# Optimization experiments

Hardware: AMD Instinct MI355X
Metric: run time of the kernel (lower is better)

## Reference

```python
import jax, jax.numpy as jnp
import numpy as np

EPS = 1e-5
LOGIT_DIM = 16   # 2**arity, arity=4
HID = 128        # circuit_hidden_dim == pe_dim
MSG = LOGIT_DIM + HID  # 144


def layer_norm(x, scale, bias):
    mu = jnp.mean(x, axis=-1, keepdims=True)
    var = jnp.mean(jnp.square(x - mu), axis=-1, keepdims=True)
    return (x - mu) * jax.lax.rsqrt(var + EPS) * scale + bias


def setup_inputs() -> dict:
    key = jax.random.key(0)
    N = 200000
    ks = jax.random.split(key, 16)
    inp = {
        'logits': jax.random.normal(ks[0], (N, LOGIT_DIM), jnp.float32),
        'hidden': jax.random.normal(ks[1], (N, HID), jnp.float32),
        'layer_pe': jax.random.normal(ks[2], (N, HID), jnp.float32),
        'intra_layer_pe': jax.random.normal(ks[3], (N, HID), jnp.float32),
        'loss': jax.random.normal(ks[4], (N,), jnp.float32),
        'layer': jax.random.randint(ks[5], (N,), 0, 8, jnp.int32),
        'sent_attributes': jax.random.normal(ks[6], (N, MSG), jnp.float32),
    }
    # LayerNorm params (scale=1, bias=0 as flax default init)
    for name, d in [('logits', LOGIT_DIM), ('hidden', HID), ('layer_pe', HID),
                    ('intra_pe', HID), ('loss', 1), ('msg', MSG)]:
        inp[f'ln_{name}_s'] = jnp.ones((d,), jnp.float32)
        inp[f'ln_{name}_b'] = jnp.zeros((d,), jnp.float32)
    # MLP: 545 -> 256 (LN, relu) -> 256 (LN, relu) -> 144
    D_IN = LOGIT_DIM + HID + HID + HID + 1 + MSG  # 545
    inp['W0'] = jax.random.normal(ks[7], (D_IN, 256), jnp.float32) * 0.02
    inp['b0'] = jnp.zeros((256,), jnp.float32)
    inp['mlp_ln0_s'] = jnp.ones((256,), jnp.float32)
    inp['mlp_ln0_b'] = jnp.zeros((256,), jnp.float32)
    inp['W1'] = jax.random.normal(ks[8], (256, 256), jnp.float32) * 0.02
    inp['b1'] = jnp.zeros((256,), jnp.float32)
    inp['mlp_ln1_s'] = jnp.ones((256,), jnp.float32)
    inp['mlp_ln1_b'] = jnp.zeros((256,), jnp.float32)
    inp['W2'] = jax.random.normal(ks[9], (256, MSG), jnp.float32) * 0.02
    inp['b2'] = jnp.zeros((MSG,), jnp.float32)
    return inp


def reference(logits, hidden, layer_pe, intra_layer_pe, loss, layer, sent_attributes,
              ln_logits_s, ln_logits_b, ln_hidden_s, ln_hidden_b,
              ln_layer_pe_s, ln_layer_pe_b, ln_intra_pe_s, ln_intra_pe_b,
              ln_loss_s, ln_loss_b, ln_msg_s, ln_msg_b,
              W0, b0, mlp_ln0_s, mlp_ln0_b, W1, b1, mlp_ln1_s, mlp_ln1_b, W2, b2):
    # Five field-wise LayerNorms + message LayerNorm, then concat
    x = jnp.concatenate([
        layer_norm(logits, ln_logits_s, ln_logits_b),
        layer_norm(hidden, ln_hidden_s, ln_hidden_b),
        layer_norm(layer_pe, ln_layer_pe_s, ln_layer_pe_b),
        layer_norm(intra_layer_pe, ln_intra_pe_s, ln_intra_pe_b),
        layer_norm(loss[:, None], ln_loss_s, ln_loss_b),
        layer_norm(sent_attributes, ln_msg_s, ln_msg_b),
    ], axis=-1)  # [N, 545]
    # MLP: Linear + LN + relu (x2), final Linear
    h = jax.nn.relu(layer_norm(x @ W0 + b0, mlp_ln0_s, mlp_ln0_b))
    h = jax.nn.relu(layer_norm(h @ W1 + b1, mlp_ln1_s, mlp_ln1_b))
    delta = h @ W2 + b2  # [N, 144]
    delta_logits = delta[..., :LOGIT_DIM]
    delta_hidden = delta[..., LOGIT_DIM:]
    # Masked residual: only gate nodes (layer > 0) are updated; scales are 1.0
    mask = (layer > 0)[:, None]
    updated_logits = jnp.where(mask, logits + delta_logits, logits)
    updated_hidden = jnp.where(mask, hidden + delta_hidden, hidden)
    return jnp.concatenate([updated_logits, updated_hidden], axis=-1)  # [N, 144]
```

## Files before the change

### kernel.cpp

```cpp
#include <hip/hip_runtime.h>
#include <hip/hip_bf16.h>

#define EPSV 1e-5f
#define BM   32
#define XSTR 552
#define DSTR 276

using bf16x8 = __attribute__((ext_vector_type(8))) short;
using f32x4  = __attribute__((ext_vector_type(4))) float;
using us4    = __attribute__((ext_vector_type(4))) unsigned short;
using us8    = __attribute__((ext_vector_type(8))) unsigned short;

__device__ __forceinline__ unsigned short f2bf(float f) {
    unsigned int u = __float_as_uint(f);
    u += 0x7fffu + ((u >> 16) & 1u);
    return (unsigned short)(u >> 16);
}

__global__ void prep_kernel(const float* __restrict__ W0, const float* __restrict__ b0,
                            const float* __restrict__ ln_loss_b,
                            const float* __restrict__ W1, const float* __restrict__ W2,
                            unsigned short* __restrict__ W0p, unsigned short* __restrict__ W1p,
                            unsigned short* __restrict__ W2p, float* __restrict__ b0e)
{
    int gtid = blockIdx.x * blockDim.x + threadIdx.x;
    if (gtid < 17408) {
        int lane = gtid & 63, fid = gtid >> 6;
        int s = fid >> 4, t = fid & 15;
        int n  = (t << 4) + (lane & 15);
        int kb = (s << 5) + ((lane >> 4) << 3);
        us8 v;
        #pragma unroll
        for (int i = 0; i < 8; ++i) {
            int k = kb + i;
            int orig = (k < 144) ? k : ((k < 288) ? (k + 257) : (k - 144));
            v[i] = f2bf(W0[orig * 256 + n]);
        }
        *reinterpret_cast<us8*>(W0p + gtid * 8) = v;
    } else if (gtid < 17408 + 8192) {
        int g = gtid - 17408;
        int lane = g & 63, fid = g >> 6;
        int s = fid >> 4, t = fid & 15;
        int n  = (t << 4) + (lane & 15);
        int kb = (s << 5) + ((lane >> 4) << 3);
        us8 v;
        #pragma unroll
        for (int i = 0; i < 8; ++i) v[i] = f2bf(W1[(kb + i) * 256 + n]);
        *reinterpret_cast<us8*>(W1p + g * 8) = v;
    } else if (gtid < 17408 + 8192 + 4608) {
        int g = gtid - 17408 - 8192;
        int lane = g & 63, fid = g >> 6;
        int s = fid / 9, t = fid % 9;
        int n  = (t << 4) + (lane & 15);
        int kb = (s << 5) + ((lane >> 4) << 3);
        us8 v;
        #pragma unroll
        for (int i = 0; i < 8; ++i) v[i] = f2bf(W2[(kb + i) * 144 + n]);
        *reinterpret_cast<us8*>(W2p + g * 8) = v;
    } else if (gtid < 17408 + 8192 + 4608 + 256) {
        int n = gtid - (17408 + 8192 + 4608);
        b0e[n] = b0[n] + ln_loss_b[0] * W0[400 * 256 + n];
    }
}

template<int L>
__device__ __forceinline__ void stage8(
    const float* __restrict__ src,
    const float* __restrict__ sc, const float* __restrict__ bi,
    unsigned short* xb, int dstcol, int tid, int row0)
{
    constexpr int SPAN = L / 8;
    const int sub = tid & 7;
    const int r   = tid >> 3;
    const float* p = src + (size_t)(row0 + r) * L + sub * SPAN;
    float ps = 0.f, pq = 0.f;
    if constexpr (SPAN % 4 == 0) {
        constexpr int NV = SPAN / 4;
        float4 v[NV];
        #pragma unroll
        for (int j = 0; j < NV; ++j) {
            v[j] = *reinterpret_cast<const float4*>(p + 4 * j);
            ps += v[j].x + v[j].y + v[j].z + v[j].w;
            pq += v[j].x * v[j].x + v[j].y * v[j].y + v[j].z * v[j].z + v[j].w * v[j].w;
        }
        ps += __shfl_xor(ps, 1); ps += __shfl_xor(ps, 2); ps += __shfl_xor(ps, 4);
        pq += __shfl_xor(pq, 1); pq += __shfl_xor(pq, 2); pq += __shfl_xor(pq, 4);
        const float mu   = ps * (1.f / L);
        const float rstd = rsqrtf(pq * (1.f / L) - mu * mu + EPSV);
        unsigned short* dst = xb + r * XSTR + dstcol + sub * SPAN;
        const float* scp = sc + sub * SPAN;
        const float* bip = bi + sub * SPAN;
        #pragma unroll
        for (int j = 0; j < NV; ++j) {
            float4 sv = *reinterpret_cast<const float4*>(scp + 4 * j);
            float4 bv = *reinterpret_cast<const float4*>(bip + 4 * j);
            us4 o;
            o[0] = f2bf((v[j].x - mu) * rstd * sv.x + bv.x);
            o[1] = f2bf((v[j].y - mu) * rstd * sv.y + bv.y);
            o[2] = f2bf((v[j].z - mu) * rstd * sv.z + bv.z);
            o[3] = f2bf((v[j].w - mu) * rstd * sv.w + bv.w);
            *reinterpret_cast<us4*>(dst + 4 * j) = o;
        }
    } else {
        constexpr int NV = SPAN / 2;
        float2 v[NV];
        #pragma unroll
        for (int j = 0; j < NV; ++j) {
            v[j] = *reinterpret_cast<const float2*>(p + 2 * j);
            ps += v[j].x + v[j].y;
            pq += v[j].x * v[j].x + v[j].y * v[j].y;
        }
        ps += __shfl_xor(ps, 1); ps += __shfl_xor(ps, 2); ps += __shfl_xor(ps, 4);
        pq += __shfl_xor(pq, 1); pq += __shfl_xor(pq, 2); pq += __shfl_xor(pq, 4);
        const float mu   = ps * (1.f / L);
        const float rstd = rsqrtf(pq * (1.f / L) - mu * mu + EPSV);
        unsigned short* dst = xb + r * XSTR + dstcol + sub * SPAN;
        const float* scp = sc + sub * SPAN;
        const float* bip = bi + sub * SPAN;
        #pragma unroll
        for (int j = 0; j < NV; ++j) {
            float2 sv = *reinterpret_cast<const float2*>(scp + 2 * j);
            float2 bv = *reinterpret_cast<const float2*>(bip + 2 * j);
            unsigned int pk = (unsigned int)f2bf((v[j].x - mu) * rstd * sv.x + bv.x)
                            | ((unsigned int)f2bf((v[j].y - mu) * rstd * sv.y + bv.y) << 16);
            *reinterpret_cast<unsigned int*>(dst + 2 * j) = pk;
        }
    }
}

__global__ __launch_bounds__(256, 4) void node_update_kernel(
    const float* __restrict__ logits, const float* __restrict__ hidden,
    const float* __restrict__ layer_pe, const float* __restrict__ intra,
    const int* __restrict__ layer, const float* __restrict__ msg,
    const float* __restrict__ ln_logits_s, const float* __restrict__ ln_logits_b,
    const float* __restrict__ ln_hidden_s, const float* __restrict__ ln_hidden_b,
    const float* __restrict__ ln_layer_pe_s, const float* __restrict__ ln_layer_pe_b,
    const float* __restrict__ ln_intra_pe_s, const float* __restrict__ ln_intra_pe_b,
    const float* __restrict__ ln_msg_s, const float* __restrict__ ln_msg_b,
    const unsigned short* __restrict__ W0p, const float* __restrict__ b0e,
    const float* __restrict__ mlp_ln0_s, const float* __restrict__ mlp_ln0_b,
    const unsigned short* __restrict__ W1p, const float* __restrict__ b1,
    const float* __restrict__ mlp_ln1_s, const float* __restrict__ mlp_ln1_b,
    const unsigned short* __restrict__ W2p, const float* __restrict__ b2,
    float* __restrict__ out)
{
    __shared__ __align__(16) unsigned short sbuf[BM * XSTR];
    __shared__ __align__(16) float redf[BM * 4 * 2];
    __shared__ int lyr[BM];

    float2* redp = reinterpret_cast<float2*>(redf);
    const int tid  = threadIdx.x;
    const int lane = tid & 63;
    const int w    = tid >> 6;
    const int l15  = lane & 15;
    const int lg   = lane >> 4;
    const int row0 = blockIdx.x * BM;

    stage8<16 >(logits,   ln_logits_s,   ln_logits_b,   sbuf,   0, tid, row0);
    __builtin_amdgcn_sched_barrier(0);
    stage8<128>(hidden,   ln_hidden_s,   ln_hidden_b,   sbuf,  16, tid, row0);
    __builtin_amdgcn_sched_barrier(0);
    stage8<144>(msg,      ln_msg_s,      ln_msg_b,      sbuf, 144, tid, row0);
    __builtin_amdgcn_sched_barrier(0);
    stage8<128>(layer_pe, ln_layer_pe_s, ln_layer_pe_b, sbuf, 288, tid, row0);
    __builtin_amdgcn_sched_barrier(0);
    stage8<128>(intra,    ln_intra_pe_s, ln_intra_pe_b, sbuf, 416, tid, row0);
    __builtin_amdgcn_sched_barrier(0);
    if (tid < BM) lyr[tid] = layer[row0 + tid];
    __syncthreads();

    f32x4 acc[2][4];
    #pragma unroll
    for (int m = 0; m < 2; ++m)
        #pragma unroll
        for (int t = 0; t < 4; ++t)
            acc[m][t] = (f32x4){0.f, 0.f, 0.f, 0.f};

    for (int s = 0; s < 17; ++s) {
        bf16x8 a[2];
        #pragma unroll
        for (int m = 0; m < 2; ++m)
            a[m] = *reinterpret_cast<const bf16x8*>(&sbuf[(16 * m + l15) * XSTR + 32 * s + 8 * lg]);
        #pragma unroll
        for (int t = 0; t < 4; ++t) {
            bf16x8 b = *reinterpret_cast<const bf16x8*>(W0p + (((s * 16 + w * 4 + t) * 64 + lane) << 3));
            #pragma unroll
            for (int m = 0; m < 2; ++m)
                acc[m][t] = __builtin_amdgcn_mfma_f32_16x16x32_bf16(a[m], b, acc[m][t], 0, 0, 0);
        }
    }

    {
        float bv[4], sv[4], bb[4];
        #pragma unroll
        for (int t = 0; t < 4; ++t) {
            int n = w * 64 + t * 16 + l15;
            bv[t] = b0e[n]; sv[t] = mlp_ln0_s[n]; bb[t] = mlp_ln0_b[n];
        }
        #pragma unroll
        for (int m = 0; m < 2; ++m)
            #pragma unroll
            for (int t = 0; t < 4; ++t)
                #pragma unroll
                for (int i = 0; i < 4; ++i)
                    acc[m][t][i] += bv[t];
        #pragma unroll
        for (int m = 0; m < 2; ++m) {
            #pragma unroll
            for (int i = 0; i < 4; ++i) {
                float ps = acc[m][0][i] + acc[m][1][i] + acc[m][2][i] + acc[m][3][i];
                float pq = acc[m][0][i] * acc[m][0][i] + acc[m][1][i] * acc[m][1][i]
                         + acc[m][2][i] * acc[m][2][i] + acc[m][3][i] * acc[m][3][i];
                ps += __shfl_xor(ps, 1); ps += __shfl_xor(ps, 2); ps += __shfl_xor(ps, 4); ps += __shfl_xor(ps, 8);
                pq += __shfl_xor(pq, 1); pq += __shfl_xor(pq, 2); pq += __shfl_xor(pq, 4); pq += __shfl_xor(pq, 8);
                if (l15 == 0) redp[(16 * m + 4 * lg + i) * 4 + w] = make_float2(ps, pq);
            }
        }
        __syncthreads();
        if (tid < BM) {
            float2 a0 = redp[tid * 4 + 0], a1 = redp[tid * 4 + 1], a2 = redp[tid * 4 + 2], a3 = redp[tid * 4 + 3];
            float s  = a0.x + a1.x + a2.x + a3.x;
            float q  = a0.y + a1.y + a2.y + a3.y;
            float mu = s * (1.f / 256.f);
            float rstd = rsqrtf(q * (1.f / 256.f) - mu * mu + EPSV);
            redp[tid * 4 + 0] = make_float2(mu, rstd);
        }
        __syncthreads();
        #pragma unroll
        for (int m = 0; m < 2; ++m)
            #pragma unroll
            for (int i = 0; i < 4; ++i) {
                int r = 16 * m + 4 * lg + i;
                float2 mr = redp[r * 4];
                #pragma unroll
                for (int t = 0; t < 4; ++t) {
                    float y = (acc[m][t][i] - mr.x) * mr.y * sv[t] + bb[t];
                    sbuf[r * XSTR + w * 64 + t * 16 + l15] = f2bf(fmaxf(y, 0.f));
                }
            }
    }
    __syncthreads();

    #pragma unroll
    for (int m = 0; m < 2; ++m)
        #pragma unroll
        for (int t = 0; t < 4; ++t)
            acc[m][t] = (f32x4){0.f, 0.f, 0.f, 0.f};
    for (int s = 0; s < 8; ++s) {
        bf16x8 a[2];
        #pragma unroll
        for (int m = 0; m < 2; ++m)
            a[m] = *reinterpret_cast<const bf16x8*>(&sbuf[(16 * m + l15) * XSTR + 32 * s + 8 * lg]);
        #pragma unroll
        for (int t = 0; t < 4; ++t) {
            bf16x8 b = *reinterpret_cast<const bf16x8*>(W1p + (((s * 16 + w * 4 + t) * 64 + lane) << 3));
            #pragma unroll
            for (int m = 0; m < 2; ++m)
                acc[m][t] = __builtin_amdgcn_mfma_f32_16x16x32_bf16(a[m], b, acc[m][t], 0, 0, 0);
        }
    }

    {
        float bv[4], sv[4], bb[4];
        #pragma unroll
        for (int t = 0; t < 4; ++t) {
            int n = w * 64 + t * 16 + l15;
            bv[t] = b1[n]; sv[t] = mlp_ln1_s[n]; bb[t] = mlp_ln1_b[n];
        }
        #pragma unroll
        for (int m = 0; m < 2; ++m)
            #pragma unroll
            for (int t = 0; t < 4; ++t)
                #pragma unroll
                for (int i = 0; i < 4; ++i)
                    acc[m][t][i] += bv[t];
        #pragma unroll
        for (int m = 0; m < 2; ++m) {
            #pragma unroll
            for (int i = 0; i < 4; ++i) {
                float ps = acc[m][0][i] + acc[m][1][i] + acc[m][2][i] + acc[m][3][i];
                float pq = acc[m][0][i] * acc[m][0][i] + acc[m][1][i] * acc[m][1][i]
                         + acc[m][2][i] * acc[m][2][i] + acc[m][3][i] * acc[m][3][i];
                ps += __shfl_xor(ps, 1); ps += __shfl_xor(ps, 2); ps += __shfl_xor(ps, 4); ps += __shfl_xor(ps, 8);
                pq += __shfl_xor(pq, 1); pq += __shfl_xor(pq, 2); pq += __shfl_xor(pq, 4); pq += __shfl_xor(pq, 8);
                if (l15 == 0) redp[(16 * m + 4 * lg + i) * 4 + w] = make_float2(ps, pq);
            }
        }
        __syncthreads();
        if (tid < BM) {
            float2 a0 = redp[tid * 4 + 0], a1 = redp[tid * 4 + 1], a2 = redp[tid * 4 + 2], a3 = redp[tid * 4 + 3];
            float s  = a0.x + a1.x + a2.x + a3.x;
            float q  = a0.y + a1.y + a2.y + a3.y;
            float mu = s * (1.f / 256.f);
            float rstd = rsqrtf(q * (1.f / 256.f) - mu * mu + EPSV);
            redp[tid * 4 + 0] = make_float2(mu, rstd);
        }
        __syncthreads();
        #pragma unroll
        for (int m = 0; m < 2; ++m)
            #pragma unroll
            for (int i = 0; i < 4; ++i) {
                int r = 16 * m + 4 * lg + i;
                float2 mr = redp[r * 4];
                #pragma unroll
                for (int t = 0; t < 4; ++t) {
                    float y = (acc[m][t][i] - mr.x) * mr.y * sv[t] + bb[t];
                    sbuf[r * XSTR + w * 64 + t * 16 + l15] = f2bf(fmaxf(y, 0.f));
                }
            }
    }
    __syncthreads();

    {
        const int rg = w & 1;
        const int ch = w >> 1;
        const unsigned short* arow = sbuf + (16 * rg + l15) * XSTR;
        float* delta = reinterpret_cast<float*>(sbuf);
        if (ch == 0) {
            f32x4 acc3[5];
            #pragma unroll
            for (int t = 0; t < 5; ++t) acc3[t] = (f32x4){0.f, 0.f, 0.f, 0.f};
            for (int s = 0; s < 8; ++s) {
                bf16x8 a = *reinterpret_cast<const bf16x8*>(arow + 32 * s + 8 * lg);
                #pragma unroll
                for (int t = 0; t < 5; ++t) {
                    bf16x8 b = *reinterpret_cast<const bf16x8*>(W2p + (((s * 9 + t) * 64 + lane) << 3));
                    acc3[t] = __builtin_amdgcn_mfma_f32_16x16x32_bf16(a, b, acc3[t], 0, 0, 0);
                }
            }
            __syncthreads();
            #pragma unroll
            for (int t = 0; t < 5; ++t)
                #pragma unroll
                for (int i = 0; i < 4; ++i)
                    delta[(16 * rg + 4 * lg + i) * DSTR + 16 * t + l15] = acc3[t][i];
        } else {
            f32x4 acc3[4];
            #pragma unroll
            for (int t = 0; t < 4; ++t) acc3[t] = (f32x4){0.f, 0.f, 0.f, 0.f};
            for (int s = 0; s < 8; ++s) {
                bf16x8 a = *reinterpret_cast<const bf16x8*>(arow + 32 * s + 8 * lg);
                #pragma unroll
                for (int t = 0; t < 4; ++t) {
                    bf16x8 b = *reinterpret_cast<const bf16x8*>(W2p + (((s * 9 + t + 5) * 64 + lane) << 3));
                    acc3[t] = __builtin_amdgcn_mfma_f32_16x16x32_bf16(a, b, acc3[t], 0, 0, 0);
                }
            }
            __syncthreads();
            #pragma unroll
            for (int t = 0; t < 4; ++t)
                #pragma unroll
                for (int i = 0; i < 4; ++i)
                    delta[(16 * rg + 4 * lg + i) * DSTR + 16 * (t + 5) + l15] = acc3[t][i];
        }
    }
    __syncthreads();

    const float* delta = reinterpret_cast<const float*>(sbuf);
    #pragma unroll
    for (int j = 0; j < 5; ++j) {
        int idx = tid + j * 256;
        if (idx < BM * 36) {
            int r = idx / 36, c4 = idx % 36;
            int grow = row0 + r;
            float4 d  = *reinterpret_cast<const float4*>(delta + r * DSTR + 4 * c4);
            float4 bb = *reinterpret_cast<const float4*>(b2 + 4 * c4);
            float4 base;
            if (c4 < 4) base = *reinterpret_cast<const float4*>(logits + (size_t)grow * 16 + 4 * c4);
            else        base = *reinterpret_cast<const float4*>(hidden + (size_t)grow * 128 + 4 * c4 - 16);
            const bool mk = lyr[r] > 0;
            float4 o;
            o.x = mk ? base.x + d.x + bb.x : base.x;
            o.y = mk ? base.y + d.y + bb.y : base.y;
            o.z = mk ? base.z + d.z + bb.z : base.z;
            o.w = mk ? base.w + d.w + bb.w : base.w;
            *reinterpret_cast<float4*>(out + (size_t)grow * 144 + 4 * c4) = o;
        }
    }
}

extern "C" void kernel_launch(void* const* d_in, const int* in_sizes, int n_in,
                              void* d_out, int out_size, void* d_ws, size_t ws_size,
                              hipStream_t stream)
{
    const float* logits        = (const float*)d_in[0];
    const float* hidden        = (const float*)d_in[1];
    const float* layer_pe      = (const float*)d_in[2];
    const float* intra         = (const float*)d_in[3];
    const int*   layer         = (const int*)  d_in[5];
    const float* msg           = (const float*)d_in[6];
    const float* ln_logits_s   = (const float*)d_in[7];
    const float* ln_logits_b   = (const float*)d_in[8];
    const float* ln_hidden_s   = (const float*)d_in[9];
    const float* ln_hidden_b   = (const float*)d_in[10];
    const float* ln_layer_pe_s = (const float*)d_in[11];
    const float* ln_layer_pe_b = (const float*)d_in[12];
    const float* ln_intra_pe_s = (const float*)d_in[13];
    const float* ln_intra_pe_b = (const float*)d_in[14];
    const float* ln_loss_b     = (const float*)d_in[16];
    const float* ln_msg_s      = (const float*)d_in[17];
    const float* ln_msg_b      = (const float*)d_in[18];
    const float* W0            = (const float*)d_in[19];
    const float* b0            = (const float*)d_in[20];
    const float* mlp_ln0_s     = (const float*)d_in[21];
    const float* mlp_ln0_b     = (const float*)d_in[22];
    const float* W1            = (const float*)d_in[23];
    const float* b1            = (const float*)d_in[24];
    const float* mlp_ln1_s     = (const float*)d_in[25];
    const float* mlp_ln1_b     = (const float*)d_in[26];
    const float* W2            = (const float*)d_in[27];
    const float* b2            = (const float*)d_in[28];
    float* out = (float*)d_out;

    unsigned short* W0p = (unsigned short*)d_ws;
    unsigned short* W1p = (unsigned short*)((char*)d_ws + 278528);
    unsigned short* W2p = (unsigned short*)((char*)d_ws + 409600);
    float*          b0e = (float*)((char*)d_ws + 483328);

    prep_kernel<<<119, 256, 0, stream>>>(W0, b0, ln_loss_b, W1, W2, W0p, W1p, W2p, b0e);

    const int N = in_sizes[5];
    node_update_kernel<<<N / BM, 256, 0, stream>>>(
        logits, hidden, layer_pe, intra, layer, msg,
        ln_logits_s, ln_logits_b, ln_hidden_s, ln_hidden_b,
        ln_layer_pe_s, ln_layer_pe_b, ln_intra_pe_s, ln_intra_pe_b,
        ln_msg_s, ln_msg_b,
        W0p, b0e, mlp_ln0_s, mlp_ln0_b,
        W1p, b1, mlp_ln1_s, mlp_ln1_b,
        W2p, b2, out);
}
```

Baseline: 308.7 us.

## Fold input LayerNorm affine into W0 and drop per-row stats sync

```diff
diff --git a/kernel.cpp b/kernel.cpp
--- a/kernel.cpp
+++ b/kernel.cpp
@@ -17,9 +17,27 @@
     return (unsigned short)(u >> 16);
 }
 
+__device__ __forceinline__ int orig_row(int k) {
+    return (k < 144) ? k : ((k < 288) ? (k + 257) : (k - 144));
+}
+__device__ __forceinline__ float seg_pick(int k,
+    const float* a, const float* b, const float* c, const float* d, const float* e) {
+    if (k < 16)  return a[k];
+    if (k < 144) return b[k - 16];
+    if (k < 288) return c[k - 144];
+    if (k < 416) return d[k - 288];
+    return e[k - 416];
+}
+
 __global__ void prep_kernel(const float* __restrict__ W0, const float* __restrict__ b0,
                             const float* __restrict__ ln_loss_b,
                             const float* __restrict__ W1, const float* __restrict__ W2,
+                            const float* __restrict__ ls_s, const float* __restrict__ hs_s,
+                            const float* __restrict__ ms_s, const float* __restrict__ pe_s,
+                            const float* __restrict__ in_s,
+                            const float* __restrict__ ls_b, const float* __restrict__ hs_b,
+                            const float* __restrict__ ms_b, const float* __restrict__ pe_b,
+                            const float* __restrict__ in_b,
                             unsigned short* __restrict__ W0p, unsigned short* __restrict__ W1p,
                             unsigned short* __restrict__ W2p, float* __restrict__ b0e)
 {
@@ -33,8 +51,8 @@
         #pragma unroll
         for (int i = 0; i < 8; ++i) {
             int k = kb + i;
-            int orig = (k < 144) ? k : ((k < 288) ? (k + 257) : (k - 144));
-            v[i] = f2bf(W0[orig * 256 + n]);
+            float sc = seg_pick(k, ls_s, hs_s, ms_s, pe_s, in_s);
+            v[i] = f2bf(sc * W0[orig_row(k) * 256 + n]);
         }
         *reinterpret_cast<us8*>(W0p + gtid * 8) = v;
     } else if (gtid < 17408 + 8192) {
@@ -59,14 +77,18 @@
         *reinterpret_cast<us8*>(W2p + g * 8) = v;
     } else if (gtid < 17408 + 8192 + 4608 + 256) {
         int n = gtid - (17408 + 8192 + 4608);
-        b0e[n] = b0[n] + ln_loss_b[0] * W0[400 * 256 + n];
+        float acc = b0[n] + ln_loss_b[0] * W0[400 * 256 + n];
+        for (int k = 0; k < 544; ++k) {
+            float bb = seg_pick(k, ls_b, hs_b, ms_b, pe_b, in_b);
+            acc += bb * W0[orig_row(k) * 256 + n];
+        }
+        b0e[n] = acc;
     }
 }
 
 template<int L>
 __device__ __forceinline__ void stage8(
     const float* __restrict__ src,
-    const float* __restrict__ sc, const float* __restrict__ bi,
     unsigned short* xb, int dstcol, int tid, int row0)
 {
     constexpr int SPAN = L / 8;
@@ -88,17 +110,13 @@
         const float mu   = ps * (1.f / L);
         const float rstd = rsqrtf(pq * (1.f / L) - mu * mu + EPSV);
         unsigned short* dst = xb + r * XSTR + dstcol + sub * SPAN;
-        const float* scp = sc + sub * SPAN;
-        const float* bip = bi + sub * SPAN;
         #pragma unroll
         for (int j = 0; j < NV; ++j) {
-            float4 sv = *reinterpret_cast<const float4*>(scp + 4 * j);
-            float4 bv = *reinterpret_cast<const float4*>(bip + 4 * j);
             us4 o;
-            o[0] = f2bf((v[j].x - mu) * rstd * sv.x + bv.x);
-            o[1] = f2bf((v[j].y - mu) * rstd * sv.y + bv.y);
-            o[2] = f2bf((v[j].z - mu) * rstd * sv.z + bv.z);
-            o[3] = f2bf((v[j].w - mu) * rstd * sv.w + bv.w);
+            o[0] = f2bf((v[j].x - mu) * rstd);
+            o[1] = f2bf((v[j].y - mu) * rstd);
+            o[2] = f2bf((v[j].z - mu) * rstd);
+            o[3] = f2bf((v[j].w - mu) * rstd);
             *reinterpret_cast<us4*>(dst + 4 * j) = o;
         }
     } else {
@@ -115,14 +133,10 @@
         const float mu   = ps * (1.f / L);
         const float rstd = rsqrtf(pq * (1.f / L) - mu * mu + EPSV);
         unsigned short* dst = xb + r * XSTR + dstcol + sub * SPAN;
-        const float* scp = sc + sub * SPAN;
-        const float* bip = bi + sub * SPAN;
         #pragma unroll
         for (int j = 0; j < NV; ++j) {
-            float2 sv = *reinterpret_cast<const float2*>(scp + 2 * j);
-            float2 bv = *reinterpret_cast<const float2*>(bip + 2 * j);
-            unsigned int pk = (unsigned int)f2bf((v[j].x - mu) * rstd * sv.x + bv.x)
-                            | ((unsigned int)f2bf((v[j].y - mu) * rstd * sv.y + bv.y) << 16);
+            unsigned int pk = (unsigned int)f2bf((v[j].x - mu) * rstd)
+                            | ((unsigned int)f2bf((v[j].y - mu) * rstd) << 16);
             *reinterpret_cast<unsigned int*>(dst + 2 * j) = pk;
         }
     }
@@ -132,11 +146,6 @@
     const float* __restrict__ logits, const float* __restrict__ hidden,
     const float* __restrict__ layer_pe, const float* __restrict__ intra,
     const int* __restrict__ layer, const float* __restrict__ msg,
-    const float* __restrict__ ln_logits_s, const float* __restrict__ ln_logits_b,
-    const float* __restrict__ ln_hidden_s, const float* __restrict__ ln_hidden_b,
-    const float* __restrict__ ln_layer_pe_s, const float* __restrict__ ln_layer_pe_b,
-    const float* __restrict__ ln_intra_pe_s, const float* __restrict__ ln_intra_pe_b,
-    const float* __restrict__ ln_msg_s, const float* __restrict__ ln_msg_b,
     const unsigned short* __restrict__ W0p, const float* __restrict__ b0e,
     const float* __restrict__ mlp_ln0_s, const float* __restrict__ mlp_ln0_b,
     const unsigned short* __restrict__ W1p, const float* __restrict__ b1,
@@ -149,6 +158,7 @@
     __shared__ int lyr[BM];
 
     float2* redp = reinterpret_cast<float2*>(redf);
+    const float4* redq = reinterpret_cast<const float4*>(redf);
     const int tid  = threadIdx.x;
     const int lane = tid & 63;
     const int w    = tid >> 6;
@@ -156,16 +166,11 @@
     const int lg   = lane >> 4;
     const int row0 = blockIdx.x * BM;
 
-    stage8<16 >(logits,   ln_logits_s,   ln_logits_b,   sbuf,   0, tid, row0);
-    __builtin_amdgcn_sched_barrier(0);
-    stage8<128>(hidden,   ln_hidden_s,   ln_hidden_b,   sbuf,  16, tid, row0);
-    __builtin_amdgcn_sched_barrier(0);
-    stage8<144>(msg,      ln_msg_s,      ln_msg_b,      sbuf, 144, tid, row0);
-    __builtin_amdgcn_sched_barrier(0);
-    stage8<128>(layer_pe, ln_layer_pe_s, ln_layer_pe_b, sbuf, 288, tid, row0);
-    __builtin_amdgcn_sched_barrier(0);
-    stage8<128>(intra,    ln_intra_pe_s, ln_intra_pe_b, sbuf, 416, tid, row0);
-    __builtin_amdgcn_sched_barrier(0);
+    stage8<16 >(logits,   sbuf,   0, tid, row0);
+    stage8<128>(hidden,   sbuf,  16, tid, row0);
+    stage8<144>(msg,      sbuf, 144, tid, row0);
+    stage8<128>(layer_pe, sbuf, 288, tid, row0);
+    stage8<128>(intra,    sbuf, 416, tid, row0);
     if (tid < BM) lyr[tid] = layer[row0 + tid];
     __syncthreads();
 
@@ -217,24 +222,19 @@
             }
         }
         __syncthreads();
-        if (tid < BM) {
-            float2 a0 = redp[tid * 4 + 0], a1 = redp[tid * 4 + 1], a2 = redp[tid * 4 + 2], a3 = redp[tid * 4 + 3];
-            float s  = a0.x + a1.x + a2.x + a3.x;
-            float q  = a0.y + a1.y + a2.y + a3.y;
-            float mu = s * (1.f / 256.f);
-            float rstd = rsqrtf(q * (1.f / 256.f) - mu * mu + EPSV);
-            redp[tid * 4 + 0] = make_float2(mu, rstd);
-        }
-        __syncthreads();
         #pragma unroll
         for (int m = 0; m < 2; ++m)
             #pragma unroll
             for (int i = 0; i < 4; ++i) {
                 int r = 16 * m + 4 * lg + i;
-                float2 mr = redp[r * 4];
+                float4 q0 = redq[r * 2 + 0], q1 = redq[r * 2 + 1];
+                float s  = q0.x + q0.z + q1.x + q1.z;
+                float q  = q0.y + q0.w + q1.y + q1.w;
+                float mu = s * (1.f / 256.f);
+                float rstd = rsqrtf(q * (1.f / 256.f) - mu * mu + EPSV);
                 #pragma unroll
                 for (int t = 0; t < 4; ++t) {
-                    float y = (acc[m][t][i] - mr.x) * mr.y * sv[t] + bb[t];
+                    float y = (acc[m][t][i] - mu) * rstd * sv[t] + bb[t];
                     sbuf[r * XSTR + w * 64 + t * 16 + l15] = f2bf(fmaxf(y, 0.f));
                 }
             }
@@ -287,24 +287,19 @@
             }
         }
         __syncthreads();
-        if (tid < BM) {
-            float2 a0 = redp[tid * 4 + 0], a1 = redp[tid * 4 + 1], a2 = redp[tid * 4 + 2], a3 = redp[tid * 4 + 3];
-            float s  = a0.x + a1.x + a2.x + a3.x;
-            float q  = a0.y + a1.y + a2.y + a3.y;
-            float mu = s * (1.f / 256.f);
-            float rstd = rsqrtf(q * (1.f / 256.f) - mu * mu + EPSV);
-            redp[tid * 4 + 0] = make_float2(mu, rstd);
-        }
-        __syncthreads();
         #pragma unroll
         for (int m = 0; m < 2; ++m)
             #pragma unroll
             for (int i = 0; i < 4; ++i) {
                 int r = 16 * m + 4 * lg + i;
-                float2 mr = redp[r * 4];
+                float4 q0 = redq[r * 2 + 0], q1 = redq[r * 2 + 1];
+                float s  = q0.x + q0.z + q1.x + q1.z;
+                float q  = q0.y + q0.w + q1.y + q1.w;
+                float mu = s * (1.f / 256.f);
+                float rstd = rsqrtf(q * (1.f / 256.f) - mu * mu + EPSV);
                 #pragma unroll
                 for (int t = 0; t < 4; ++t) {
-                    float y = (acc[m][t][i] - mr.x) * mr.y * sv[t] + bb[t];
+                    float y = (acc[m][t][i] - mu) * rstd * sv[t] + bb[t];
                     sbuf[r * XSTR + w * 64 + t * 16 + l15] = f2bf(fmaxf(y, 0.f));
                 }
             }
@@ -417,14 +412,14 @@
     unsigned short* W2p = (unsigned short*)((char*)d_ws + 409600);
     float*          b0e = (float*)((char*)d_ws + 483328);
 
-    prep_kernel<<<119, 256, 0, stream>>>(W0, b0, ln_loss_b, W1, W2, W0p, W1p, W2p, b0e);
+    prep_kernel<<<119, 256, 0, stream>>>(W0, b0, ln_loss_b, W1, W2,
+        ln_logits_s, ln_hidden_s, ln_msg_s, ln_layer_pe_s, ln_intra_pe_s,
+        ln_logits_b, ln_hidden_b, ln_msg_b, ln_layer_pe_b, ln_intra_pe_b,
+        W0p, W1p, W2p, b0e);
 
     const int N = in_sizes[5];
     node_update_kernel<<<N / BM, 256, 0, stream>>>(
         logits, hidden, layer_pe, intra, layer, msg,
-        ln_logits_s, ln_logits_b, ln_hidden_s, ln_hidden_b,
-        ln_layer_pe_s, ln_layer_pe_b, ln_intra_pe_s, ln_intra_pe_b,
-        ln_msg_s, ln_msg_b,
         W0p, b0e, mlp_ln0_s, mlp_ln0_b,
         W1p, b1, mlp_ln1_s, mlp_ln1_b,
         W2p, b2, out);
```

Result: slower. 397.5 us (+28.8%).
